# Kernel tuning notes

Hardware: AMD Instinct MI355X
Metric: run time of the kernel (lower is better)

The kernel has to match this reference:

```python
import jax, jax.numpy as jnp
import numpy as np

N_ATOMS = 100000
N_EDGES = 400000
ATOM_DIM = 32
BOND_DIM = 16


def setup_inputs() -> dict:
    key = jax.random.key(0)
    k1, k2, k3, k4 = jax.random.split(key, 4)
    atom_features = jax.random.normal(k1, (N_ATOMS, ATOM_DIM), dtype=jnp.float32)
    bond_features = jax.random.normal(k2, (N_EDGES, BOND_DIM), dtype=jnp.float32)
    pair_indices = jax.random.randint(k3, (N_EDGES, 2), 0, N_ATOMS, dtype=jnp.int64)
    # glorot-uniform-like scale for the kernel
    limit = np.sqrt(6.0 / (BOND_DIM + ATOM_DIM * ATOM_DIM)).astype(np.float32)
    kernel = jax.random.uniform(k4, (BOND_DIM, ATOM_DIM * ATOM_DIM), dtype=jnp.float32,
                                minval=-limit, maxval=limit)
    bias = jnp.zeros((ATOM_DIM * ATOM_DIM,), dtype=jnp.float32)
    return {"atom_features": atom_features, "bond_features": bond_features,
            "pair_indices": pair_indices, "kernel": kernel, "bias": bias}


def reference(atom_features, bond_features, pair_indices, kernel, bias):
    n_atoms, d = atom_features.shape  # d = atom_dim
    e = bond_features.shape[0]
    # per-edge transform matrices: [E, d, d]
    edge_mats = (bond_features @ kernel + bias).reshape(e, d, d)
    # gather neighbor atom features via pair_indices[:, 1]
    neighbors = atom_features[pair_indices[:, 1]]  # [E, d]
    # per-edge matvec
    transformed = jnp.einsum('eij,ej->ei', edge_mats, neighbors)  # [E, d]
    # scatter-reduce onto source atoms
    return jax.ops.segment_sum(transformed, pair_indices[:, 0], num_segments=n_atoms)
```

## Files before the change

### kernel.cpp

```cpp
#include <hip/hip_runtime.h>


typedef _Float16 half8 __attribute__((ext_vector_type(8)));
typedef _Float16 half4t __attribute__((ext_vector_type(4)));
typedef float float4v __attribute__((ext_vector_type(4)));

constexpr int NA = 100000;
constexpr int E  = 400000;
constexpr int TILES = E / 32;
constexpr int NBLK  = 768;
constexpr int HALFW = NBLK * 4 / 2;

constexpr size_t OFF_ATOMH = 0;
constexpr size_t OFF_BONDH = (size_t)NA * 32 * 2;

constexpr int NZ4 = NA * 32 / 4;
constexpr int NA4 = NA * 32 / 4;
constexpr int NB4 = E * 16 / 4;
constexpr int PREP_TOT = NZ4 + NA4 + NB4;

__global__ void k_prep(const float* __restrict__ atom,
                       const float* __restrict__ bond,
                       float4* __restrict__ outz,
                       half4t* __restrict__ atomh4,
                       half4t* __restrict__ bondh4) {
  int i = blockIdx.x * blockDim.x + threadIdx.x;
  if (i < NZ4) {
    outz[i] = make_float4(0.f, 0.f, 0.f, 0.f);
  } else if (i < NZ4 + NA4) {
    int k = i - NZ4;
    float4 v = ((const float4*)atom)[k];
    half4t hh = { (_Float16)v.x, (_Float16)v.y, (_Float16)v.z, (_Float16)v.w };
    atomh4[k] = hh;
  } else if (i < PREP_TOT) {
    int k = i - NZ4 - NA4;
    float4 v = ((const float4*)bond)[k];
    half4t hh = { (_Float16)v.x, (_Float16)v.y, (_Float16)v.z, (_Float16)v.w };
    bondh4[k] = hh;
  }
}

static __device__ inline half8 splat8(_Float16 v) {
  half8 r = {v, v, v, v, v, v, v, v};
  return r;
}

__global__ __launch_bounds__(256, 3)
void edge_fused(const _Float16* __restrict__ atomh,
                const _Float16* __restrict__ bondh,
                const int* __restrict__ pairs,
                const float* __restrict__ Kmat,
                const float* __restrict__ bias,
                float* __restrict__ out)
{
  const int tid  = threadIdx.x;
  const int lane = tid & 63;
  const int wid  = blockIdx.x * 4 + (tid >> 6);
  const int h    = wid & 1;
  const int q    = lane >> 4;
  const int el   = lane & 15;
  const int n    = el + h * 16;
  const int j0   = q * 8;

  half8 Wr[17];
  #pragma unroll
  for (int s = 0; s < 17; ++s) {
    const float* src = (s < 16) ? (Kmat + s * 1024 + n * 32 + j0)
                                : (bias + n * 32 + j0);
    half8 w;
    #pragma unroll
    for (int j = 0; j < 8; ++j) w[j] = (_Float16)src[j];
    Wr[s] = w;
  }

  const int start  = wid >> 1;
  const int stride = HALFW;
  const int2* pairs2 = (const int2*)pairs;

  auto ldpv = [&](int t) -> int2 {
    const int tc = t < TILES ? t : TILES - 1;
    int2 v = make_int2(0, 0);
    if (lane < 32) v = pairs2[tc * 32 + lane];
    return v;
  };

  int2 pv0 = ldpv(start);
  int2 pv1 = ldpv(start + stride);

  half8 nbA_c, nbB_c, bA0_c, bA1_c, bB0_c, bB1_c;
  {
    const int aA = __shfl(pv0.y, el);
    const int aB = __shfl(pv0.y, el + 16);
    nbA_c = *(const half8*)(atomh + (size_t)aA * 32 + j0);
    nbB_c = *(const half8*)(atomh + (size_t)aB * 32 + j0);
    const _Float16* brA = bondh + (size_t)(start * 32 + el) * 16;
    const _Float16* brB = bondh + (size_t)(start * 32 + el + 16) * 16;
    bA0_c = *(const half8*)(brA);  bA1_c = *(const half8*)(brA + 8);
    bB0_c = *(const half8*)(brB);  bB1_c = *(const half8*)(brB + 8);
  }

  for (int t = start; t < TILES; t += stride) {
    const int tn = t + stride;

    half8 nbA_n, nbB_n, bA0_n, bA1_n, bB0_n, bB1_n;
    {
      const int aA = __shfl(pv1.y, el);
      const int aB = __shfl(pv1.y, el + 16);
      nbA_n = *(const half8*)(atomh + (size_t)aA * 32 + j0);
      nbB_n = *(const half8*)(atomh + (size_t)aB * 32 + j0);
      const int tc = tn < TILES ? tn : TILES - 1;
      const _Float16* brA = bondh + (size_t)(tc * 32 + el) * 16;
      const _Float16* brB = bondh + (size_t)(tc * 32 + el + 16) * 16;
      bA0_n = *(const half8*)(brA);  bA1_n = *(const half8*)(brA + 8);
      bB0_n = *(const half8*)(brB);  bB1_n = *(const half8*)(brB + 8);
    }
    const int2 pv2 = ldpv(tn + stride);

    float4v acc0 = {0.f, 0.f, 0.f, 0.f};
    float4v acc1 = {0.f, 0.f, 0.f, 0.f};
    #pragma unroll
    for (int s = 0; s < 16; ++s) {
      const _Float16 sA = (s < 8) ? bA0_c[s] : bA1_c[s - 8];
      const _Float16 sB = (s < 8) ? bB0_c[s] : bB1_c[s - 8];
      const half8 aAf = nbA_c * splat8(sA);
      const half8 aBf = nbB_c * splat8(sB);
      acc0 = __builtin_amdgcn_mfma_f32_16x16x32_f16(aAf, Wr[s], acc0, 0, 0, 0);
      acc1 = __builtin_amdgcn_mfma_f32_16x16x32_f16(aBf, Wr[s], acc1, 0, 0, 0);
    }
    acc0 = __builtin_amdgcn_mfma_f32_16x16x32_f16(nbA_c, Wr[16], acc0, 0, 0, 0);
    acc1 = __builtin_amdgcn_mfma_f32_16x16x32_f16(nbB_c, Wr[16], acc1, 0, 0, 0);

    #pragma unroll
    for (int r = 0; r < 4; ++r) {
      const int s0 = __shfl(pv0.x, q * 4 + r);
      atomicAdd(out + (size_t)s0 * 32 + n, acc0[r]);
      const int s1 = __shfl(pv0.x, q * 4 + r + 16);
      atomicAdd(out + (size_t)s1 * 32 + n, acc1[r]);
    }

    pv0 = pv1; pv1 = pv2;
    nbA_c = nbA_n; nbB_c = nbB_n;
    bA0_c = bA0_n; bA1_c = bA1_n; bB0_c = bB0_n; bB1_c = bB1_n;
  }
}

extern "C" void kernel_launch(void* const* d_in, const int* in_sizes, int n_in,
                              void* d_out, int out_size, void* d_ws, size_t ws_size,
                              hipStream_t stream) {
  const float* atom  = (const float*)d_in[0];
  const float* bondf = (const float*)d_in[1];
  const int*   pairs = (const int*)d_in[2];
  const float* Kmat  = (const float*)d_in[3];
  const float* bias  = (const float*)d_in[4];
  float* out = (float*)d_out;

  _Float16* atomh = (_Float16*)((char*)d_ws + OFF_ATOMH);
  _Float16* bondh = (_Float16*)((char*)d_ws + OFF_BONDH);

  k_prep<<<(PREP_TOT + 255) / 256, 256, 0, stream>>>(
      atom, bondf, (float4*)out, (half4t*)atomh, (half4t*)bondh);
  edge_fused<<<NBLK, 256, 0, stream>>>(atomh, bondh, pairs, Kmat, bias, out);
}
```

Before: 141.7 us.

## Counting-sort edges by destination and merge same-destination atomics in registers

Adds a counting sort of edges by destination atom, built from a histogram, a two-level scan and a scatter, and moves the bond fp16 conversion into the scatter. The edge kernel then reads the sorted pairs and bonds, remaps lanes so each lane's accumulator rows cover consecutive edges, and folds contributions to the same destination before issuing atomicAdd. The aim is fewer global atomics. The cost is four extra kernel launches plus an atomic histogram and scatter pass over all edges. With random destinations at about 4 edges per atom, runs of equal destinations inside an 8-edge group are short, so the saving may be small.

```diff
diff --git a/kernel.cpp b/kernel.cpp
--- a/kernel.cpp
+++ b/kernel.cpp
@@ -10,21 +10,26 @@
 constexpr int TILES = E / 32;
 constexpr int NBLK  = 768;
 constexpr int HALFW = NBLK * 4 / 2;
+constexpr int NCHUNK = (NA + 1023) / 1024;
 
 constexpr size_t OFF_ATOMH = 0;
-constexpr size_t OFF_BONDH = (size_t)NA * 32 * 2;
+constexpr size_t OFF_BONDS = (size_t)NA * 32 * 2;
+constexpr size_t OFF_PAIRS = OFF_BONDS + (size_t)E*16*2;
+constexpr size_t OFF_HIST  = OFF_PAIRS + (size_t)E*8;
+constexpr size_t OFF_BASE  = OFF_HIST + (size_t)NA*4;
+constexpr size_t OFF_BSUM  = OFF_BASE + (size_t)NA*4;
+constexpr size_t OFF_BOFF  = OFF_BSUM + 512;
 
 constexpr int NZ4 = NA * 32 / 4;
 constexpr int NA4 = NA * 32 / 4;
-constexpr int NB4 = E * 16 / 4;
-constexpr int PREP_TOT = NZ4 + NA4 + NB4;
-
-__global__ void k_prep(const float* __restrict__ atom,
-                       const float* __restrict__ bond,
-                       float4* __restrict__ outz,
-                       half4t* __restrict__ atomh4,
-                       half4t* __restrict__ bondh4) {
-  int i = blockIdx.x * blockDim.x + threadIdx.x;
+constexpr int NH4 = NA / 4;
+constexpr int K0_TOT = NZ4 + NA4 + NH4;
+
+__global__ void k_zero_conv(const float* __restrict__ atom,
+                            float4* __restrict__ outz,
+                            half4t* __restrict__ atomh4,
+                            uint4* __restrict__ histz) {
+  int i = blockIdx.x * 256 + threadIdx.x;
   if (i < NZ4) {
     outz[i] = make_float4(0.f, 0.f, 0.f, 0.f);
   } else if (i < NZ4 + NA4) {
@@ -32,12 +37,84 @@
     float4 v = ((const float4*)atom)[k];
     half4t hh = { (_Float16)v.x, (_Float16)v.y, (_Float16)v.z, (_Float16)v.w };
     atomh4[k] = hh;
-  } else if (i < PREP_TOT) {
+  } else if (i < K0_TOT) {
     int k = i - NZ4 - NA4;
-    float4 v = ((const float4*)bond)[k];
-    half4t hh = { (_Float16)v.x, (_Float16)v.y, (_Float16)v.z, (_Float16)v.w };
-    bondh4[k] = hh;
-  }
+    histz[k] = make_uint4(0u, 0u, 0u, 0u);
+  }
+}
+
+__global__ void k_hist(const int2* __restrict__ pairs2,
+                       unsigned* __restrict__ hist) {
+  int e = blockIdx.x * 256 + threadIdx.x;
+  if (e >= E) return;
+  atomicAdd(&hist[(unsigned)pairs2[e].x], 1u);
+}
+
+__global__ void k_scan_chunks(const unsigned* __restrict__ hist,
+                              unsigned* __restrict__ base,
+                              unsigned* __restrict__ bsum) {
+  __shared__ unsigned s[256];
+  const int t  = threadIdx.x;
+  const int i0 = blockIdx.x * 1024 + t * 4;
+  unsigned c[4], sum = 0;
+  #pragma unroll
+  for (int j = 0; j < 4; ++j) {
+    unsigned v = (i0 + j < NA) ? hist[i0 + j] : 0u;
+    c[j] = v; sum += v;
+  }
+  s[t] = sum;
+  __syncthreads();
+  for (int off = 1; off < 256; off <<= 1) {
+    unsigned v = (t >= off) ? s[t - off] : 0u;
+    __syncthreads();
+    s[t] += v;
+    __syncthreads();
+  }
+  if (t == 255) bsum[blockIdx.x] = s[255];
+  unsigned run = (t == 0) ? 0u : s[t - 1];
+  #pragma unroll
+  for (int j = 0; j < 4; ++j) {
+    if (i0 + j < NA) base[i0 + j] = run;
+    run += c[j];
+  }
+}
+
+__global__ void k_scan_tops(const unsigned* __restrict__ bsum,
+                            unsigned* __restrict__ boff) {
+  __shared__ unsigned s[128];
+  const int t = threadIdx.x;
+  s[t] = (t < NCHUNK) ? bsum[t] : 0u;
+  __syncthreads();
+  for (int off = 1; off < 128; off <<= 1) {
+    unsigned v = (t >= off) ? s[t - off] : 0u;
+    __syncthreads();
+    s[t] += v;
+    __syncthreads();
+  }
+  if (t < NCHUNK) boff[t] = (t == 0) ? 0u : s[t - 1];
+}
+
+__global__ void k_scatter(const int2* __restrict__ pairs2,
+                          const float4* __restrict__ bondf4,
+                          unsigned* __restrict__ hist,
+                          const unsigned* __restrict__ base,
+                          const unsigned* __restrict__ boff,
+                          int2* __restrict__ pairs_s,
+                          half8* __restrict__ bondh_s) {
+  int e = blockIdx.x * 256 + threadIdx.x;
+  if (e >= E) return;
+  int2 p = pairs2[e];
+  unsigned d = (unsigned)p.x;
+  unsigned pos = base[d] + boff[d >> 10] + (atomicSub(&hist[d], 1u) - 1u);
+  pairs_s[pos] = p;
+  float4 b0 = bondf4[e * 4 + 0], b1 = bondf4[e * 4 + 1];
+  float4 b2 = bondf4[e * 4 + 2], b3 = bondf4[e * 4 + 3];
+  half8 h0 = { (_Float16)b0.x, (_Float16)b0.y, (_Float16)b0.z, (_Float16)b0.w,
+               (_Float16)b1.x, (_Float16)b1.y, (_Float16)b1.z, (_Float16)b1.w };
+  half8 h1 = { (_Float16)b2.x, (_Float16)b2.y, (_Float16)b2.z, (_Float16)b2.w,
+               (_Float16)b3.x, (_Float16)b3.y, (_Float16)b3.z, (_Float16)b3.w };
+  bondh_s[(size_t)pos * 2 + 0] = h0;
+  bondh_s[(size_t)pos * 2 + 1] = h1;
 }
 
 static __device__ inline half8 splat8(_Float16 v) {
@@ -46,12 +123,12 @@
 }
 
 __global__ __launch_bounds__(256, 3)
-void edge_fused(const _Float16* __restrict__ atomh,
-                const _Float16* __restrict__ bondh,
-                const int* __restrict__ pairs,
-                const float* __restrict__ Kmat,
-                const float* __restrict__ bias,
-                float* __restrict__ out)
+void edge_sorted(const _Float16* __restrict__ atomh,
+                 const _Float16* __restrict__ bondh,
+                 const int* __restrict__ pairs_s,
+                 const float* __restrict__ Kmat,
+                 const float* __restrict__ bias,
+                 float* __restrict__ out)
 {
   const int tid  = threadIdx.x;
   const int lane = tid & 63;
@@ -61,6 +138,7 @@
   const int el   = lane & 15;
   const int n    = el + h * 16;
   const int j0   = q * 8;
+  const int eA   = ((el >> 2) * 8) + (el & 3);
 
   half8 Wr[17];
   #pragma unroll
@@ -75,7 +153,7 @@
 
   const int start  = wid >> 1;
   const int stride = HALFW;
-  const int2* pairs2 = (const int2*)pairs;
+  const int2* pairs2 = (const int2*)pairs_s;
 
   auto ldpv = [&](int t) -> int2 {
     const int tc = t < TILES ? t : TILES - 1;
@@ -89,12 +167,12 @@
 
   half8 nbA_c, nbB_c, bA0_c, bA1_c, bB0_c, bB1_c;
   {
-    const int aA = __shfl(pv0.y, el);
-    const int aB = __shfl(pv0.y, el + 16);
+    const int aA = __shfl(pv0.y, eA);
+    const int aB = __shfl(pv0.y, eA + 4);
     nbA_c = *(const half8*)(atomh + (size_t)aA * 32 + j0);
     nbB_c = *(const half8*)(atomh + (size_t)aB * 32 + j0);
-    const _Float16* brA = bondh + (size_t)(start * 32 + el) * 16;
-    const _Float16* brB = bondh + (size_t)(start * 32 + el + 16) * 16;
+    const _Float16* brA = bondh + (size_t)(start * 32 + eA) * 16;
+    const _Float16* brB = bondh + (size_t)(start * 32 + eA + 4) * 16;
     bA0_c = *(const half8*)(brA);  bA1_c = *(const half8*)(brA + 8);
     bB0_c = *(const half8*)(brB);  bB1_c = *(const half8*)(brB + 8);
   }
@@ -104,13 +182,13 @@
 
     half8 nbA_n, nbB_n, bA0_n, bA1_n, bB0_n, bB1_n;
     {
-      const int aA = __shfl(pv1.y, el);
-      const int aB = __shfl(pv1.y, el + 16);
+      const int aA = __shfl(pv1.y, eA);
+      const int aB = __shfl(pv1.y, eA + 4);
       nbA_n = *(const half8*)(atomh + (size_t)aA * 32 + j0);
       nbB_n = *(const half8*)(atomh + (size_t)aB * 32 + j0);
       const int tc = tn < TILES ? tn : TILES - 1;
-      const _Float16* brA = bondh + (size_t)(tc * 32 + el) * 16;
-      const _Float16* brB = bondh + (size_t)(tc * 32 + el + 16) * 16;
+      const _Float16* brA = bondh + (size_t)(tc * 32 + eA) * 16;
+      const _Float16* brB = bondh + (size_t)(tc * 32 + eA + 4) * 16;
       bA0_n = *(const half8*)(brA);  bA1_n = *(const half8*)(brA + 8);
       bB0_n = *(const half8*)(brB);  bB1_n = *(const half8*)(brB + 8);
     }
@@ -130,12 +208,21 @@
     acc0 = __builtin_amdgcn_mfma_f32_16x16x32_f16(nbA_c, Wr[16], acc0, 0, 0, 0);
     acc1 = __builtin_amdgcn_mfma_f32_16x16x32_f16(nbB_c, Wr[16], acc1, 0, 0, 0);
 
-    #pragma unroll
-    for (int r = 0; r < 4; ++r) {
-      const int s0 = __shfl(pv0.x, q * 4 + r);
-      atomicAdd(out + (size_t)s0 * 32 + n, acc0[r]);
-      const int s1 = __shfl(pv0.x, q * 4 + r + 16);
-      atomicAdd(out + (size_t)s1 * 32 + n, acc1[r]);
+    {
+      int   cur = __shfl(pv0.x, q * 8);
+      float run = acc0[0];
+      #pragma unroll
+      for (int m = 1; m < 8; ++m) {
+        const float v  = (m < 4) ? acc0[m] : acc1[m - 4];
+        const int   dm = __shfl(pv0.x, q * 8 + m);
+        if (dm == cur) {
+          run += v;
+        } else {
+          atomicAdd(out + (size_t)cur * 32 + n, run);
+          run = v; cur = dm;
+        }
+      }
+      atomicAdd(out + (size_t)cur * 32 + n, run);
     }
 
     pv0 = pv1; pv1 = pv2;
@@ -154,10 +241,23 @@
   const float* bias  = (const float*)d_in[4];
   float* out = (float*)d_out;
 
-  _Float16* atomh = (_Float16*)((char*)d_ws + OFF_ATOMH);
-  _Float16* bondh = (_Float16*)((char*)d_ws + OFF_BONDH);
-
-  k_prep<<<(PREP_TOT + 255) / 256, 256, 0, stream>>>(
-      atom, bondf, (float4*)out, (half4t*)atomh, (half4t*)bondh);
-  edge_fused<<<NBLK, 256, 0, stream>>>(atomh, bondh, pairs, Kmat, bias, out);
-}
+  char* ws = (char*)d_ws;
+  _Float16* atomh   = (_Float16*)(ws + OFF_ATOMH);
+  _Float16* bondh_s = (_Float16*)(ws + OFF_BONDS);
+  int2*     pairs_s = (int2*)    (ws + OFF_PAIRS);
+  unsigned* hist    = (unsigned*)(ws + OFF_HIST);
+  unsigned* base    = (unsigned*)(ws + OFF_BASE);
+  unsigned* bsum    = (unsigned*)(ws + OFF_BSUM);
+  unsigned* boff    = (unsigned*)(ws + OFF_BOFF);
+
+  k_zero_conv<<<(K0_TOT + 255) / 256, 256, 0, stream>>>(
+      atom, (float4*)out, (half4t*)atomh, (uint4*)hist);
+  k_hist<<<(E + 255) / 256, 256, 0, stream>>>((const int2*)pairs, hist);
+  k_scan_chunks<<<NCHUNK, 256, 0, stream>>>(hist, base, bsum);
+  k_scan_tops<<<1, 128, 0, stream>>>(bsum, boff);
+  k_scatter<<<(E + 255) / 256, 256, 0, stream>>>(
+      (const int2*)pairs, (const float4*)bondf, hist, base, boff,
+      pairs_s, (half8*)bondh_s);
+  edge_sorted<<<NBLK, 256, 0, stream>>>(
+      atomh, bondh_s, (const int*)pairs_s, Kmat, bias, out);
+}
```

After: 171.8 us. 1.21x slower.

## Accumulate scatter in fp16 via packed half2 atomics, then convert to fp32

Applied to the files above, without the earlier changes.

Replaces the per-element fp32 atomicAdd scatter with packed __half2 atomics into an fp16 workspace accumulator. Adjacent lanes are combined with a shuffle so only half the lanes issue atomics, and a new finalize kernel converts the fp16 accumulator to the fp32 output. The aim is to halve the atomic count and the scatter traffic. In exchange it adds an extra kernel launch and pass over the output, and accumulating sums in fp16 risks precision loss and overflow.

```diff
diff --git a/kernel.cpp b/kernel.cpp
--- a/kernel.cpp
+++ b/kernel.cpp
@@ -1,4 +1,5 @@
 #include <hip/hip_runtime.h>
+#include <hip/hip_fp16.h>
 
 
 typedef _Float16 half8 __attribute__((ext_vector_type(8)));
@@ -13,6 +14,7 @@
 
 constexpr size_t OFF_ATOMH = 0;
 constexpr size_t OFF_BONDH = (size_t)NA * 32 * 2;
+constexpr size_t OFF_ACC   = OFF_BONDH + (size_t)E*16*2;
 
 constexpr int NZ4 = NA * 32 / 4;
 constexpr int NA4 = NA * 32 / 4;
@@ -21,12 +23,13 @@
 
 __global__ void k_prep(const float* __restrict__ atom,
                        const float* __restrict__ bond,
-                       float4* __restrict__ outz,
+                       half4t* __restrict__ accz,
                        half4t* __restrict__ atomh4,
                        half4t* __restrict__ bondh4) {
-  int i = blockIdx.x * blockDim.x + threadIdx.x;
+  int i = blockIdx.x * 256 + threadIdx.x;
   if (i < NZ4) {
-    outz[i] = make_float4(0.f, 0.f, 0.f, 0.f);
+    half4t z = { (_Float16)0.f, (_Float16)0.f, (_Float16)0.f, (_Float16)0.f };
+    accz[i] = z;
   } else if (i < NZ4 + NA4) {
     int k = i - NZ4;
     float4 v = ((const float4*)atom)[k];
@@ -51,7 +54,7 @@
                 const int* __restrict__ pairs,
                 const float* __restrict__ Kmat,
                 const float* __restrict__ bias,
-                float* __restrict__ out)
+                _Float16* __restrict__ accum)
 {
   const int tid  = threadIdx.x;
   const int lane = tid & 63;
@@ -132,16 +135,42 @@
 
     #pragma unroll
     for (int r = 0; r < 4; ++r) {
-      const int s0 = __shfl(pv0.x, q * 4 + r);
-      atomicAdd(out + (size_t)s0 * 32 + n, acc0[r]);
-      const int s1 = __shfl(pv0.x, q * 4 + r + 16);
-      atomicAdd(out + (size_t)s1 * 32 + n, acc1[r]);
+      {
+        const int   s0 = __shfl(pv0.x, q * 4 + r);
+        const float v  = acc0[r];
+        const float pvx = __shfl_xor(v, 1);
+        if (!(el & 1)) {
+          union { _Float16 f[2]; __half2 h; } u;
+          u.f[0] = (_Float16)v; u.f[1] = (_Float16)pvx;
+          unsafeAtomicAdd(
+              reinterpret_cast<__half2*>(accum + (size_t)s0 * 32 + n), u.h);
+        }
+      }
+      {
+        const int   s1 = __shfl(pv0.x, q * 4 + r + 16);
+        const float v  = acc1[r];
+        const float pvx = __shfl_xor(v, 1);
+        if (!(el & 1)) {
+          union { _Float16 f[2]; __half2 h; } u;
+          u.f[0] = (_Float16)v; u.f[1] = (_Float16)pvx;
+          unsafeAtomicAdd(
+              reinterpret_cast<__half2*>(accum + (size_t)s1 * 32 + n), u.h);
+        }
+      }
     }
 
     pv0 = pv1; pv1 = pv2;
     nbA_c = nbA_n; nbB_c = nbB_n;
     bA0_c = bA0_n; bA1_c = bA1_n; bB0_c = bB0_n; bB1_c = bB1_n;
   }
+}
+
+__global__ void k_fin(const half4t* __restrict__ acc4,
+                      float4* __restrict__ out4) {
+  int i = blockIdx.x * 256 + threadIdx.x;
+  if (i >= NZ4) return;
+  half4t v = acc4[i];
+  out4[i] = make_float4((float)v[0], (float)v[1], (float)v[2], (float)v[3]);
 }
 
 extern "C" void kernel_launch(void* const* d_in, const int* in_sizes, int n_in,
@@ -154,10 +183,14 @@
   const float* bias  = (const float*)d_in[4];
   float* out = (float*)d_out;
 
-  _Float16* atomh = (_Float16*)((char*)d_ws + OFF_ATOMH);
-  _Float16* bondh = (_Float16*)((char*)d_ws + OFF_BONDH);
+  char* ws = (char*)d_ws;
+  _Float16* atomh = (_Float16*)(ws + OFF_ATOMH);
+  _Float16* bondh = (_Float16*)(ws + OFF_BONDH);
+  _Float16* accum = (_Float16*)(ws + OFF_ACC);
 
   k_prep<<<(PREP_TOT + 255) / 256, 256, 0, stream>>>(
-      atom, bondf, (float4*)out, (half4t*)atomh, (half4t*)bondh);
-  edge_fused<<<NBLK, 256, 0, stream>>>(atomh, bondh, pairs, Kmat, bias, out);
+      atom, bondf, (half4t*)accum, (half4t*)atomh, (half4t*)bondh);
+  edge_fused<<<NBLK, 256, 0, stream>>>(atomh, bondh, pairs, Kmat, bias, accum);
+  k_fin<<<(NZ4 + 255) / 256, 256, 0, stream>>>((const half4t*)accum,
+                                               (float4*)out);
 }
```

After: 146.7 us. +3.5%, slower.
